# Kernel tuning notes

Hardware: AMD Instinct MI355X
Metric: run time of the kernel (lower is better)

Reference implementation:

```python
import jax, jax.numpy as jnp
import numpy as np

EPS = 1e-06  # used both as eps and as the F.threshold threshold (mqjs passes eps as th)


def _pair_log_dist_sum(x1, x2, th):
    # dist[i,j] = ||x1_i||^2 + ||x2_j||^2 - 2 x1_i . x2_j  (n x n)
    x1x2 = x1 @ x2.T
    sq1 = jnp.sum(x1 * x1, axis=1)[:, None]
    sq2 = jnp.sum(x2 * x2, axis=1)[None, :]
    dist = sq1 + sq2 - 2.0 * x1x2
    # F.threshold(dist, th, 1): values <= th -> 1; then clamp(min=1), sqrt, log, row-sum
    dist = jnp.where(dist > th, dist, 1.0)
    dist = jnp.maximum(dist, 1.0)
    return jnp.sum(0.5 * jnp.log(dist), axis=1)  # log(sqrt(d)) == 0.5*log(d)


def _mqjs(inp, tgt, eps):
    n = inp.shape[0]
    x1 = inp.reshape(n, -1)
    x2 = tgt.reshape(n, -1)
    p = (x1 + x2) / 2.0
    ce = _pair_log_dist_sum(x1, p, eps) + _pair_log_dist_sum(x2, p, eps)
    se = _pair_log_dist_sum(x1, x1, eps) * (n / (n - 1))
    return jnp.mean(ce - se)


def setup_inputs() -> dict:
    key = jax.random.key(0)
    k1, k2 = jax.random.split(key)
    n, d = 8192, 256
    inp = jax.random.normal(k1, (n, d), dtype=jnp.float32)
    tgt = jax.random.normal(k2, (n, d), dtype=jnp.float32)
    return {"input": inp, "target": tgt}


def reference(input, target):
    return _mqjs(input, target, EPS)
```

## Files before the change

kernel.cpp:

```cpp
#include <hip/hip_runtime.h>

#define N 8192
#define D 256
#define BM 128
#define JG 4
#define GJ (N / BM / JG)
#define GI (N / BM)
#define NBLK (GJ * GI)

typedef int   i32x4 __attribute__((ext_vector_type(4)));
typedef int   i32x8 __attribute__((ext_vector_type(8)));
typedef float f32x4 __attribute__((ext_vector_type(4)));

__device__ __forceinline__ unsigned pack_fp8x4(float a, float b, float c, float d) {
    unsigned lo = __builtin_amdgcn_cvt_pk_fp8_f32(a, b, 0, false);
    return __builtin_amdgcn_cvt_pk_fp8_f32(c, d, lo, true);
}
__device__ __forceinline__ float dequant_sumsq(unsigned q) {
    const float v0 = __builtin_amdgcn_cvt_f32_fp8(q, 0);
    const float v1 = __builtin_amdgcn_cvt_f32_fp8(q, 1);
    const float v2 = __builtin_amdgcn_cvt_f32_fp8(q, 2);
    const float v3 = __builtin_amdgcn_cvt_f32_fp8(q, 3);
    return fmaf(v0, v0, fmaf(v1, v1, fmaf(v2, v2, v3 * v3)));
}

__global__ void prep_kernel(const float* __restrict__ x1, const float* __restrict__ x2,
                            unsigned* __restrict__ x1q, unsigned* __restrict__ x2q,
                            unsigned* __restrict__ pq,
                            float* __restrict__ sq1, float* __restrict__ sq2,
                            float* __restrict__ sqp) {
    const int tid = threadIdx.x, lane = tid & 63, wv = tid >> 6;
    const int rowbase = blockIdx.x * 16 + wv * 4;
    for (int r = 0; r < 4; ++r) {
        const int row = rowbase + r;
        const size_t eb = (size_t)row * D + lane * 4;
        const float4 a = *(const float4*)(x1 + eb);
        const float4 b = *(const float4*)(x2 + eb);
        const float px = 0.5f * (a.x + b.x), py = 0.5f * (a.y + b.y);
        const float pz = 0.5f * (a.z + b.z), pw = 0.5f * (a.w + b.w);
        const unsigned qa = pack_fp8x4(a.x, a.y, a.z, a.w);
        const unsigned qb = pack_fp8x4(b.x, b.y, b.z, b.w);
        const unsigned qp = pack_fp8x4(px, py, pz, pw);
        const size_t wb = (size_t)row * (D / 4) + lane;
        x1q[wb] = qa; x2q[wb] = qb; pq[wb] = qp;
        float s1 = dequant_sumsq(qa), s2 = dequant_sumsq(qb), sp = dequant_sumsq(qp);
        #pragma unroll
        for (int o = 32; o > 0; o >>= 1) {
            s1 += __shfl_down(s1, o, 64);
            s2 += __shfl_down(s2, o, 64);
            sp += __shfl_down(sp, o, 64);
        }
        if (lane == 0) { sq1[row] = s1; sq2[row] = s2; sqp[row] = sp; }
    }
}

__device__ __forceinline__ f32x4 mfma8(i32x8 a, i32x8 b, f32x4 c) {
    return __builtin_amdgcn_mfma_scale_f32_16x16x128_f8f6f4(
        a, b, c, 0, 0, 0, 0x7F7F7F7F, 0, 0x7F7F7F7F);
}

__device__ __forceinline__ i32x8 read_frag(const unsigned char* Ts, int m, int quad) {
    const int r7 = m & 7;
    const i32x4 lo = *(const i32x4*)(Ts + m * 128 + ((((2 * quad)     ^ r7)) << 4));
    const i32x4 hi = *(const i32x4*)(Ts + m * 128 + ((((2 * quad + 1) ^ r7)) << 4));
    i32x8 f;
    f[0] = lo[0]; f[1] = lo[1]; f[2] = lo[2]; f[3] = lo[3];
    f[4] = hi[0]; f[5] = hi[1]; f[6] = hi[2]; f[7] = hi[3];
    return f;
}

__device__ __forceinline__ void stage_tile(const unsigned char* __restrict__ g,
                                           unsigned char* s, int rowbase, size_t kb,
                                           int wv, int srow, int sblk) {
    #pragma unroll
    for (int it = 0; it < 4; ++it) {
        const int grp = wv * 4 + it;
        const int row = grp * 8 + srow;
        __builtin_amdgcn_global_load_lds(
            (const __attribute__((address_space(1))) void*)(g + (size_t)(rowbase + row) * D + kb + sblk * 16),
            (__attribute__((address_space(3))) void*)(s + grp * 1024), 16, 0, 0);
    }
}

__device__ __forceinline__ float tile_logsum(const f32x4 (&acc)[4][4],
                                             const float* __restrict__ sqA_lds,
                                             const float sb[4],
                                             int wr, int quad) {
    float s = 0.0f;
    #pragma unroll
    for (int ti = 0; ti < 4; ++ti) {
        float sa[4];
        #pragma unroll
        for (int r = 0; r < 4; ++r) sa[r] = sqA_lds[wr * 64 + ti * 16 + quad * 4 + r];
        #pragma unroll
        for (int tjp = 0; tjp < 2; ++tjp) {
            float pr = 1.0f;
            #pragma unroll
            for (int tj = tjp * 2; tj < tjp * 2 + 2; ++tj)
                #pragma unroll
                for (int r = 0; r < 4; ++r) {
                    float d = fmaf(-2.0f, acc[ti][tj][r], sa[r] + sb[tj]);
                    pr *= fmaxf(d, 1.0f);
                }
            s += __logf(pr);
        }
    }
    return s;
}

__global__ __launch_bounds__(256, 1) void mqjs_main(
    const unsigned char* __restrict__ x1q, const unsigned char* __restrict__ x2q,
    const unsigned char* __restrict__ pq,
    const float* __restrict__ sq1, const float* __restrict__ sq2,
    const float* __restrict__ sqp, float* __restrict__ partials) {

    __shared__ __align__(16) unsigned char A1s[2 * BM * 128];
    __shared__ __align__(16) unsigned char A2s[2 * BM * 128];
    __shared__ __align__(16) unsigned char BAs[2 * BM * 128];
    __shared__ __align__(16) unsigned char BBs[2 * BM * 128];
    __shared__ float sqa1[BM], sqa2[BM];
    __shared__ float red[4];

    const int tid = threadIdx.x;
    const int lane = tid & 63;
    const int wv = tid >> 6;
    const int wr = wv >> 1, wc = wv & 1;
    const int quad = lane >> 4, l15 = lane & 15;

    const int I0 = blockIdx.y * BM;
    const int jbase = blockIdx.x * JG;
    const float wse = -(float)N / (float)(N - 1);

    const int srow = lane >> 3;
    const int sblk = (lane & 7) ^ srow;

    stage_tile(x1q, A1s,         I0, 0,   wv, srow, sblk);
    stage_tile(x1q, A1s + 16384, I0, 128, wv, srow, sblk);
    stage_tile(x2q, A2s,         I0, 0,   wv, srow, sblk);
    stage_tile(x2q, A2s + 16384, I0, 128, wv, srow, sblk);
    stage_tile(pq,  BAs,         jbase * BM, 0,   wv, srow, sblk);
    stage_tile(pq,  BAs + 16384, jbase * BM, 128, wv, srow, sblk);
    if (tid < BM) sqa1[tid] = sq1[I0 + tid];
    else          sqa2[tid - BM] = sq2[I0 + tid - BM];
    if (tid >= BM) sqa1[tid - BM] = sq1[I0 + tid - BM];
    else           sqa2[tid] = sq2[I0 + tid];
    __syncthreads();

    i32x8 a1f[2][4];
    #pragma unroll
    for (int kc = 0; kc < 2; ++kc)
        #pragma unroll
        for (int ti = 0; ti < 4; ++ti)
            a1f[kc][ti] = read_frag(A1s + kc * 16384, wr * 64 + ti * 16 + l15, quad);

    float tsum = 0.0f;

    for (int jj = 0; jj < JG; ++jj) {
        const int J0 = (jbase + jj) * BM;
        const bool doSym = (J0 >= I0);

        f32x4 acc0[4][4], acc1[4][4];
        #pragma unroll
        for (int a = 0; a < 4; ++a)
            #pragma unroll
            for (int b = 0; b < 4; ++b) {
                acc0[a][b] = (f32x4){0.f, 0.f, 0.f, 0.f};
                acc1[a][b] = (f32x4){0.f, 0.f, 0.f, 0.f};
            }
        #pragma unroll
        for (int kc = 0; kc < 2; ++kc) {
            i32x8 bfr[4];
            #pragma unroll
            for (int tj = 0; tj < 4; ++tj)
                bfr[tj] = read_frag(BAs + kc * 16384, wc * 64 + tj * 16 + l15, quad);
            #pragma unroll
            for (int ti = 0; ti < 4; ++ti) {
                const i32x8 a2 = read_frag(A2s + kc * 16384, wr * 64 + ti * 16 + l15, quad);
                #pragma unroll
                for (int tj = 0; tj < 4; ++tj) {
                    acc0[ti][tj] = mfma8(a1f[kc][ti], bfr[tj], acc0[ti][tj]);
                    acc1[ti][tj] = mfma8(a2,          bfr[tj], acc1[ti][tj]);
                }
            }
        }

        if (doSym) {
            stage_tile(x1q, BBs,         J0, 0,   wv, srow, sblk);
            stage_tile(x1q, BBs + 16384, J0, 128, wv, srow, sblk);
        }

        {
            float sbp[4];
            #pragma unroll
            for (int tj = 0; tj < 4; ++tj) sbp[tj] = sqp[J0 + wc * 64 + tj * 16 + l15];
            tsum += 0.5f * tile_logsum(acc0, sqa1, sbp, wr, quad);
            tsum += 0.5f * tile_logsum(acc1, sqa2, sbp, wr, quad);
        }
        __syncthreads();

        f32x4 acc2[4][4];
        if (doSym) {
            #pragma unroll
            for (int a = 0; a < 4; ++a)
                #pragma unroll
                for (int b = 0; b < 4; ++b)
                    acc2[a][b] = (f32x4){0.f, 0.f, 0.f, 0.f};
            #pragma unroll
            for (int kc = 0; kc < 2; ++kc) {
                i32x8 bfr[4];
                #pragma unroll
                for (int tj = 0; tj < 4; ++tj)
                    bfr[tj] = read_frag(BBs + kc * 16384, wc * 64 + tj * 16 + l15, quad);
                #pragma unroll
                for (int ti = 0; ti < 4; ++ti)
                    #pragma unroll
                    for (int tj = 0; tj < 4; ++tj)
                        acc2[ti][tj] = mfma8(a1f[kc][ti], bfr[tj], acc2[ti][tj]);
            }
        }

        if (jj < JG - 1) {
            stage_tile(pq, BAs,         (jbase + jj + 1) * BM, 0,   wv, srow, sblk);
            stage_tile(pq, BAs + 16384, (jbase + jj + 1) * BM, 128, wv, srow, sblk);
        }

        if (doSym) {
            float sbx[4];
            #pragma unroll
            for (int tj = 0; tj < 4; ++tj) sbx[tj] = sq1[J0 + wc * 64 + tj * 16 + l15];
            const float wg = (I0 == J0) ? wse : 2.0f * wse;
            tsum += (0.5f * wg) * tile_logsum(acc2, sqa1, sbx, wr, quad);
        }
        __syncthreads();
    }

    #pragma unroll
    for (int o = 32; o > 0; o >>= 1) tsum += __shfl_down(tsum, o, 64);
    if (lane == 0) red[wv] = tsum;
    __syncthreads();
    if (tid == 0)
        partials[blockIdx.y * GJ + blockIdx.x] = red[0] + red[1] + red[2] + red[3];
}

__global__ void finalize_kernel(const float* __restrict__ partials, float* __restrict__ out) {
    const int tid = threadIdx.x;
    const float4 v = ((const float4*)partials)[tid];
    double s = (double)v.x + (double)v.y + (double)v.z + (double)v.w;
    #pragma unroll
    for (int o = 32; o > 0; o >>= 1) s += __shfl_down(s, o, 64);
    __shared__ double r[4];
    if ((tid & 63) == 0) r[tid >> 6] = s;
    __syncthreads();
    if (tid == 0) out[0] = (float)((r[0] + r[1] + r[2] + r[3]) / (double)N);
}

extern "C" void kernel_launch(void* const* d_in, const int* in_sizes, int n_in,
                              void* d_out, int out_size, void* d_ws, size_t ws_size,
                              hipStream_t stream) {
    const float* x1 = (const float*)d_in[0];
    const float* x2 = (const float*)d_in[1];

    char* ws = (char*)d_ws;
    const size_t MBYTES = (size_t)N * D;
    unsigned* x1q = (unsigned*)(ws);
    unsigned* x2q = (unsigned*)(ws + MBYTES);
    unsigned* pq  = (unsigned*)(ws + 2 * MBYTES);
    float* sq1 = (float*)(ws + 3 * MBYTES);
    float* sq2 = (float*)(ws + 3 * MBYTES + (size_t)N * 4);
    float* sqp = (float*)(ws + 3 * MBYTES + (size_t)N * 8);
    float* partials = (float*)(ws + 3 * MBYTES + (size_t)N * 12);

    prep_kernel<<<N / 16, 256, 0, stream>>>(x1, x2, x1q, x2q, pq, sq1, sq2, sqp);
    mqjs_main<<<dim3(GJ, GI), 256, 0, stream>>>(
        (const unsigned char*)x1q, (const unsigned char*)x2q, (const unsigned char*)pq,
        sq1, sq2, sqp, partials);
    finalize_kernel<<<1, 256, 0, stream>>>(partials, (float*)d_out);
}
```

Before: 149.5 us.

## Shrink column tiles, reuse A LDS buffer, raise occupancy, refine symmetric diagonal

Column tiles narrow from 128 to 64 rows and each block walks 8 of them, which halves the accumulator register footprint. The launch bound no longer forces one block per CU. The x1 A-tile is read into registers and its LDS buffer is then refilled with x2, cutting shared memory so more blocks can be resident. Diagonal-straddling symmetric tiles now apply element-wise j>i / j>=i masking rather than whole-tile weights, and the log-sum is written with packed float2 math. The prep kernel now handles one row per wave. The risk is extra per-tile sync and B-tile staging overhead from the smaller tiles.

```diff
diff --git a/kernel.cpp b/kernel.cpp
--- a/kernel.cpp
+++ b/kernel.cpp
@@ -3,14 +3,15 @@
 #define N 8192
 #define D 256
 #define BM 128
-#define JG 4
-#define GJ (N / BM / JG)
+#define BJ 64
+#define JG 8
+#define GJ (N / BJ / JG)
 #define GI (N / BM)
-#define NBLK (GJ * GI)
 
 typedef int   i32x4 __attribute__((ext_vector_type(4)));
 typedef int   i32x8 __attribute__((ext_vector_type(8)));
 typedef float f32x4 __attribute__((ext_vector_type(4)));
+typedef float f32x2 __attribute__((ext_vector_type(2)));
 
 __device__ __forceinline__ unsigned pack_fp8x4(float a, float b, float c, float d) {
     unsigned lo = __builtin_amdgcn_cvt_pk_fp8_f32(a, b, 0, false);
@@ -30,28 +31,25 @@
                             float* __restrict__ sq1, float* __restrict__ sq2,
                             float* __restrict__ sqp) {
     const int tid = threadIdx.x, lane = tid & 63, wv = tid >> 6;
-    const int rowbase = blockIdx.x * 16 + wv * 4;
-    for (int r = 0; r < 4; ++r) {
-        const int row = rowbase + r;
-        const size_t eb = (size_t)row * D + lane * 4;
-        const float4 a = *(const float4*)(x1 + eb);
-        const float4 b = *(const float4*)(x2 + eb);
-        const float px = 0.5f * (a.x + b.x), py = 0.5f * (a.y + b.y);
-        const float pz = 0.5f * (a.z + b.z), pw = 0.5f * (a.w + b.w);
-        const unsigned qa = pack_fp8x4(a.x, a.y, a.z, a.w);
-        const unsigned qb = pack_fp8x4(b.x, b.y, b.z, b.w);
-        const unsigned qp = pack_fp8x4(px, py, pz, pw);
-        const size_t wb = (size_t)row * (D / 4) + lane;
-        x1q[wb] = qa; x2q[wb] = qb; pq[wb] = qp;
-        float s1 = dequant_sumsq(qa), s2 = dequant_sumsq(qb), sp = dequant_sumsq(qp);
-        #pragma unroll
-        for (int o = 32; o > 0; o >>= 1) {
-            s1 += __shfl_down(s1, o, 64);
-            s2 += __shfl_down(s2, o, 64);
-            sp += __shfl_down(sp, o, 64);
-        }
-        if (lane == 0) { sq1[row] = s1; sq2[row] = s2; sqp[row] = sp; }
-    }
+    const int row = blockIdx.x * 4 + wv;
+    const size_t eb = (size_t)row * D + lane * 4;
+    const float4 a = *(const float4*)(x1 + eb);
+    const float4 b = *(const float4*)(x2 + eb);
+    const float px = 0.5f * (a.x + b.x), py = 0.5f * (a.y + b.y);
+    const float pz = 0.5f * (a.z + b.z), pw = 0.5f * (a.w + b.w);
+    const unsigned qa = pack_fp8x4(a.x, a.y, a.z, a.w);
+    const unsigned qb = pack_fp8x4(b.x, b.y, b.z, b.w);
+    const unsigned qp = pack_fp8x4(px, py, pz, pw);
+    const size_t wb = (size_t)row * (D / 4) + lane;
+    x1q[wb] = qa; x2q[wb] = qb; pq[wb] = qp;
+    float s1 = dequant_sumsq(qa), s2 = dequant_sumsq(qb), sp = dequant_sumsq(qp);
+    #pragma unroll
+    for (int o = 32; o > 0; o >>= 1) {
+        s1 += __shfl_down(s1, o, 64);
+        s2 += __shfl_down(s2, o, 64);
+        sp += __shfl_down(sp, o, 64);
+    }
+    if (lane == 0) { sq1[row] = s1; sq2[row] = s2; sqp[row] = sp; }
 }
 
 __device__ __forceinline__ f32x4 mfma8(i32x8 a, i32x8 b, f32x4 c) {
@@ -69,9 +67,9 @@
     return f;
 }
 
-__device__ __forceinline__ void stage_tile(const unsigned char* __restrict__ g,
-                                           unsigned char* s, int rowbase, size_t kb,
-                                           int wv, int srow, int sblk) {
+__device__ __forceinline__ void stageA(const unsigned char* __restrict__ g,
+                                       unsigned char* s, int rowbase, size_t kb,
+                                       int wv, int srow, int sblk) {
     #pragma unroll
     for (int it = 0; it < 4; ++it) {
         const int grp = wv * 4 + it;
@@ -81,43 +79,83 @@
             (__attribute__((address_space(3))) void*)(s + grp * 1024), 16, 0, 0);
     }
 }
-
-__device__ __forceinline__ float tile_logsum(const f32x4 (&acc)[4][4],
-                                             const float* __restrict__ sqA_lds,
-                                             const float sb[4],
-                                             int wr, int quad) {
+__device__ __forceinline__ void stageB(const unsigned char* __restrict__ g,
+                                       unsigned char* s, int rowbase, size_t kb,
+                                       int wv, int srow, int sblk) {
+    #pragma unroll
+    for (int it = 0; it < 2; ++it) {
+        const int grp = wv * 2 + it;
+        const int row = grp * 8 + srow;
+        __builtin_amdgcn_global_load_lds(
+            (const __attribute__((address_space(1))) void*)(g + (size_t)(rowbase + row) * D + kb + sblk * 16),
+            (__attribute__((address_space(3))) void*)(s + grp * 1024), 16, 0, 0);
+    }
+}
+
+__device__ __forceinline__ float logsumP(const f32x4 (&acc)[4][2],
+                                         const float* __restrict__ sqA,
+                                         const float sb[2], int wr, int quad) {
     float s = 0.0f;
     #pragma unroll
     for (int ti = 0; ti < 4; ++ti) {
-        float sa[4];
-        #pragma unroll
-        for (int r = 0; r < 4; ++r) sa[r] = sqA_lds[wr * 64 + ti * 16 + quad * 4 + r];
-        #pragma unroll
-        for (int tjp = 0; tjp < 2; ++tjp) {
+        const int base = wr * 64 + ti * 16 + quad * 4;
+        const f32x2 sa01 = {sqA[base], sqA[base + 1]};
+        const f32x2 sa23 = {sqA[base + 2], sqA[base + 3]};
+        f32x2 pr = {1.0f, 1.0f};
+        #pragma unroll
+        for (int tj = 0; tj < 2; ++tj) {
+            const f32x2 sbv = {sb[tj], sb[tj]};
+            const f32x2 t01 = sa01 + sbv, t23 = sa23 + sbv;
+            const f32x2 v01 = {acc[ti][tj][0], acc[ti][tj][1]};
+            const f32x2 v23 = {acc[ti][tj][2], acc[ti][tj][3]};
+            f32x2 d01 = t01 - 2.0f * v01;
+            f32x2 d23 = t23 - 2.0f * v23;
+            d01 = __builtin_elementwise_max(d01, (f32x2){1.0f, 1.0f});
+            d23 = __builtin_elementwise_max(d23, (f32x2){1.0f, 1.0f});
+            pr *= d01; pr *= d23;
+        }
+        s += __logf(pr.x * pr.y);
+    }
+    return s;
+}
+
+__device__ __forceinline__ float logsumStraddle(const f32x4 (&acc)[4][2],
+                                                const float* __restrict__ sqA,
+                                                const float sb[2],
+                                                int wr, int wc, int quad, int l15,
+                                                int I0, int J0) {
+    float s = 0.0f;
+    #pragma unroll
+    for (int ti = 0; ti < 4; ++ti) {
+        #pragma unroll
+        for (int tj = 0; tj < 2; ++tj) {
+            const int j = J0 + wc * 32 + tj * 16 + l15;
             float pr = 1.0f;
             #pragma unroll
-            for (int tj = tjp * 2; tj < tjp * 2 + 2; ++tj)
-                #pragma unroll
-                for (int r = 0; r < 4; ++r) {
-                    float d = fmaf(-2.0f, acc[ti][tj][r], sa[r] + sb[tj]);
-                    pr *= fmaxf(d, 1.0f);
-                }
+            for (int r = 0; r < 4; ++r) {
+                const int i = I0 + wr * 64 + ti * 16 + quad * 4 + r;
+                float d = fmaf(-2.0f, acc[ti][tj][r],
+                               sqA[wr * 64 + ti * 16 + quad * 4 + r] + sb[tj]);
+                d = fmaxf(d, 1.0f);
+                const float t = (j > i) ? d : 1.0f;
+                const float u = (j >= i) ? d : 1.0f;
+                pr *= t * u;
+            }
             s += __logf(pr);
         }
     }
     return s;
 }
 
-__global__ __launch_bounds__(256, 1) void mqjs_main(
+__global__ __launch_bounds__(256) void mqjs_main(
     const unsigned char* __restrict__ x1q, const unsigned char* __restrict__ x2q,
     const unsigned char* __restrict__ pq,
     const float* __restrict__ sq1, const float* __restrict__ sq2,
     const float* __restrict__ sqp, float* __restrict__ partials) {
 
-    __shared__ __align__(16) unsigned char A1s[2 * BM * 128];
     __shared__ __align__(16) unsigned char A2s[2 * BM * 128];
-    __shared__ __align__(16) unsigned char BAs[2 * BM * 128];
-    __shared__ __align__(16) unsigned char BBs[2 * BM * 128];
+    __shared__ __align__(16) unsigned char BAs[2 * BJ * 128];
+    __shared__ __align__(16) unsigned char BBs[2 * BJ * 128];
     __shared__ float sqa1[BM], sqa2[BM];
     __shared__ float red[4];
 
@@ -134,16 +172,12 @@
     const int srow = lane >> 3;
     const int sblk = (lane & 7) ^ srow;
 
-    stage_tile(x1q, A1s,         I0, 0,   wv, srow, sblk);
-    stage_tile(x1q, A1s + 16384, I0, 128, wv, srow, sblk);
-    stage_tile(x2q, A2s,         I0, 0,   wv, srow, sblk);
-    stage_tile(x2q, A2s + 16384, I0, 128, wv, srow, sblk);
-    stage_tile(pq,  BAs,         jbase * BM, 0,   wv, srow, sblk);
-    stage_tile(pq,  BAs + 16384, jbase * BM, 128, wv, srow, sblk);
+    stageA(x1q, A2s,         I0, 0,   wv, srow, sblk);
+    stageA(x1q, A2s + 16384, I0, 128, wv, srow, sblk);
+    stageB(pq,  BAs,         jbase * BJ, 0,   wv, srow, sblk);
+    stageB(pq,  BAs + 8192,  jbase * BJ, 128, wv, srow, sblk);
     if (tid < BM) sqa1[tid] = sq1[I0 + tid];
     else          sqa2[tid - BM] = sq2[I0 + tid - BM];
-    if (tid >= BM) sqa1[tid - BM] = sq1[I0 + tid - BM];
-    else           sqa2[tid] = sq2[I0 + tid];
     __syncthreads();
 
     i32x8 a1f[2][4];
@@ -151,33 +185,38 @@
     for (int kc = 0; kc < 2; ++kc)
         #pragma unroll
         for (int ti = 0; ti < 4; ++ti)
-            a1f[kc][ti] = read_frag(A1s + kc * 16384, wr * 64 + ti * 16 + l15, quad);
+            a1f[kc][ti] = read_frag(A2s + kc * 16384, wr * 64 + ti * 16 + l15, quad);
+    __syncthreads();
+    stageA(x2q, A2s,         I0, 0,   wv, srow, sblk);
+    stageA(x2q, A2s + 16384, I0, 128, wv, srow, sblk);
+    __syncthreads();
 
     float tsum = 0.0f;
 
     for (int jj = 0; jj < JG; ++jj) {
-        const int J0 = (jbase + jj) * BM;
+        const int J0 = (jbase + jj) * BJ;
         const bool doSym = (J0 >= I0);
-
-        f32x4 acc0[4][4], acc1[4][4];
+        const bool full  = (J0 >= I0 + BM);
+
+        f32x4 acc0[4][2], acc1[4][2];
         #pragma unroll
         for (int a = 0; a < 4; ++a)
             #pragma unroll
-            for (int b = 0; b < 4; ++b) {
+            for (int b = 0; b < 2; ++b) {
                 acc0[a][b] = (f32x4){0.f, 0.f, 0.f, 0.f};
                 acc1[a][b] = (f32x4){0.f, 0.f, 0.f, 0.f};
             }
         #pragma unroll
         for (int kc = 0; kc < 2; ++kc) {
-            i32x8 bfr[4];
-            #pragma unroll
-            for (int tj = 0; tj < 4; ++tj)
-                bfr[tj] = read_frag(BAs + kc * 16384, wc * 64 + tj * 16 + l15, quad);
+            i32x8 bfr[2];
+            #pragma unroll
+            for (int tj = 0; tj < 2; ++tj)
+                bfr[tj] = read_frag(BAs + kc * 8192, wc * 32 + tj * 16 + l15, quad);
             #pragma unroll
             for (int ti = 0; ti < 4; ++ti) {
                 const i32x8 a2 = read_frag(A2s + kc * 16384, wr * 64 + ti * 16 + l15, quad);
                 #pragma unroll
-                for (int tj = 0; tj < 4; ++tj) {
+                for (int tj = 0; tj < 2; ++tj) {
                     acc0[ti][tj] = mfma8(a1f[kc][ti], bfr[tj], acc0[ti][tj]);
                     acc1[ti][tj] = mfma8(a2,          bfr[tj], acc1[ti][tj]);
                 }
@@ -185,51 +224,53 @@
         }
 
         if (doSym) {
-            stage_tile(x1q, BBs,         J0, 0,   wv, srow, sblk);
-            stage_tile(x1q, BBs + 16384, J0, 128, wv, srow, sblk);
+            stageB(x1q, BBs,        J0, 0,   wv, srow, sblk);
+            stageB(x1q, BBs + 8192, J0, 128, wv, srow, sblk);
         }
 
         {
-            float sbp[4];
-            #pragma unroll
-            for (int tj = 0; tj < 4; ++tj) sbp[tj] = sqp[J0 + wc * 64 + tj * 16 + l15];
-            tsum += 0.5f * tile_logsum(acc0, sqa1, sbp, wr, quad);
-            tsum += 0.5f * tile_logsum(acc1, sqa2, sbp, wr, quad);
+            float sbp[2];
+            #pragma unroll
+            for (int tj = 0; tj < 2; ++tj) sbp[tj] = sqp[J0 + wc * 32 + tj * 16 + l15];
+            tsum += 0.5f * logsumP(acc0, sqa1, sbp, wr, quad);
+            tsum += 0.5f * logsumP(acc1, sqa2, sbp, wr, quad);
         }
         __syncthreads();
 
-        f32x4 acc2[4][4];
+        f32x4 acc2[4][2];
         if (doSym) {
             #pragma unroll
             for (int a = 0; a < 4; ++a)
                 #pragma unroll
-                for (int b = 0; b < 4; ++b)
+                for (int b = 0; b < 2; ++b)
                     acc2[a][b] = (f32x4){0.f, 0.f, 0.f, 0.f};
             #pragma unroll
             for (int kc = 0; kc < 2; ++kc) {
-                i32x8 bfr[4];
+                i32x8 bfr[2];
                 #pragma unroll
-                for (int tj = 0; tj < 4; ++tj)
-                    bfr[tj] = read_frag(BBs + kc * 16384, wc * 64 + tj * 16 + l15, quad);
+                for (int tj = 0; tj < 2; ++tj)
+                    bfr[tj] = read_frag(BBs + kc * 8192, wc * 32 + tj * 16 + l15, quad);
                 #pragma unroll
                 for (int ti = 0; ti < 4; ++ti)
                     #pragma unroll
-                    for (int tj = 0; tj < 4; ++tj)
+                    for (int tj = 0; tj < 2; ++tj)
                         acc2[ti][tj] = mfma8(a1f[kc][ti], bfr[tj], acc2[ti][tj]);
             }
         }
 
         if (jj < JG - 1) {
-            stage_tile(pq, BAs,         (jbase + jj + 1) * BM, 0,   wv, srow, sblk);
-            stage_tile(pq, BAs + 16384, (jbase + jj + 1) * BM, 128, wv, srow, sblk);
+            stageB(pq, BAs,        (jbase + jj + 1) * BJ, 0,   wv, srow, sblk);
+            stageB(pq, BAs + 8192, (jbase + jj + 1) * BJ, 128, wv, srow, sblk);
         }
 
         if (doSym) {
-            float sbx[4];
-            #pragma unroll
-            for (int tj = 0; tj < 4; ++tj) sbx[tj] = sq1[J0 + wc * 64 + tj * 16 + l15];
-            const float wg = (I0 == J0) ? wse : 2.0f * wse;
-            tsum += (0.5f * wg) * tile_logsum(acc2, sqa1, sbx, wr, quad);
+            float sbx[2];
+            #pragma unroll
+            for (int tj = 0; tj < 2; ++tj) sbx[tj] = sq1[J0 + wc * 32 + tj * 16 + l15];
+            if (full)
+                tsum += wse * logsumP(acc2, sqa1, sbx, wr, quad);
+            else
+                tsum += 0.5f * wse * logsumStraddle(acc2, sqa1, sbx, wr, wc, quad, l15, I0, J0);
         }
         __syncthreads();
     }
@@ -270,7 +311,7 @@
     float* sqp = (float*)(ws + 3 * MBYTES + (size_t)N * 8);
     float* partials = (float*)(ws + 3 * MBYTES + (size_t)N * 12);
 
-    prep_kernel<<<N / 16, 256, 0, stream>>>(x1, x2, x1q, x2q, pq, sq1, sq2, sqp);
+    prep_kernel<<<N / 4, 256, 0, stream>>>(x1, x2, x1q, x2q, pq, sq1, sq2, sqp);
     mqjs_main<<<dim3(GJ, GI), 256, 0, stream>>>(
         (const unsigned char*)x1q, (const unsigned char*)x2q, (const unsigned char*)pq,
         sq1, sq2, sqp, partials);
```

Measured after the change: 153.5 us. 2.6% more time.
